# Optimization experiments

Hardware: AMD Instinct MI355X
Metric: run time of the kernel (lower is better)

Reference implementation:

```python
import jax, jax.numpy as jnp
import numpy as np

B, S, D, H = 2, 2048, 1024, 16
DK = D // H
ROPE_BASE = 10000


def _rope_tables(seq_len, dim):
    # RotaryEmbedding.__call__: freqs [S, dim/2], emb = concat([freqs, freqs]) -> [S, dim]
    inv_freq = 1.0 / (ROPE_BASE ** (jnp.arange(0, dim, 2, dtype=jnp.float32) / dim))
    t = jnp.arange(seq_len, dtype=jnp.float32)
    freqs = jnp.outer(t, inv_freq)
    emb = jnp.concatenate([freqs, freqs], axis=-1)
    return jnp.cos(emb), jnp.sin(emb)


def _apply_rope(x, cos, sin):
    # Faithful to apply_rotary_pos_emb: interleaved even/odd channel rotation
    cos = cos[None, None, :, :]  # [1,1,S,DK]
    sin = sin[None, None, :, :]
    x1 = x[..., 0::2]
    x2 = x[..., 1::2]
    r1 = x1 * cos[..., 0::2] - x2 * sin[..., 1::2]
    r2 = x1 * sin[..., 0::2] + x2 * cos[..., 1::2]
    return jnp.stack([r1, r2], axis=-1).reshape(x.shape)


def setup_inputs() -> dict:
    key = jax.random.key(0)
    ks = jax.random.split(key, 11)
    xavier = lambda k: jax.random.uniform(k, (D, D), jnp.float32,
                                          -jnp.sqrt(6.0 / (D + D)), jnp.sqrt(6.0 / (D + D)))
    return {
        "query": jax.random.normal(ks[0], (B, S, D), jnp.float32),
        "key": jax.random.normal(ks[1], (B, S, D), jnp.float32),
        "value": jax.random.normal(ks[2], (B, S, D), jnp.float32),
        "Wq": xavier(ks[3]), "bq": jnp.zeros((D,), jnp.float32),
        "Wk": xavier(ks[4]), "bk": jnp.zeros((D,), jnp.float32),
        "Wv": xavier(ks[5]), "bv": jnp.zeros((D,), jnp.float32),
        "Wo": xavier(ks[6]), "bo": jnp.zeros((D,), jnp.float32),
    }


def reference(query, key, value, Wq, bq, Wk, bk, Wv, bv, Wo, bo):
    def split_heads(x):  # [B,S,D] -> [B,H,S,DK]
        return x.reshape(B, S, H, DK).transpose(0, 2, 1, 3)

    q = split_heads(query @ Wq + bq)
    k = split_heads(key @ Wk + bk)
    v = split_heads(value @ Wv + bv)

    cos, sin = _rope_tables(S, DK)
    q = _apply_rope(q, cos, sin)
    k = _apply_rope(k, cos, sin)

    scores = jnp.einsum("bhqd,bhkd->bhqk", q, k) / jnp.sqrt(jnp.float32(DK))
    causal = jnp.tril(jnp.ones((S, S), dtype=bool))
    scores = jnp.where(causal, scores, jnp.float32(-1e10))
    attn = jax.nn.softmax(scores, axis=-1)
    out = jnp.einsum("bhqk,bhkd->bhqd", attn, v)  # [B,H,S,DK]
    out = out.transpose(0, 2, 1, 3).reshape(B, S, D)
    return out @ Wo + bo
```

## Files before the change

### kernel.cpp

```cpp
#include <hip/hip_runtime.h>
#include <hip/hip_bf16.h>
#include <math.h>

#define B_ 2
#define S_ 2048
#define D_ 1024
#define H_ 16
#define DK_ 64

#define ROPE_C 0.4152410118609203f
#define LOG2E 1.4426950408889634f
#define QSCALE 0.18033688011112042f

typedef float f4 __attribute__((ext_vector_type(4)));
typedef short s8 __attribute__((ext_vector_type(8)));

__device__ __forceinline__ ushort f2b(float f) {
  union { float f; uint u; } v; v.f = f;
  uint u = v.u + 0x7fffu + ((v.u >> 16) & 1u);
  return (ushort)(u >> 16);
}

__device__ __forceinline__ float b2f(ushort u) {
  union { uint u; float f; } v; v.u = ((uint)u) << 16;
  return v.f;
}

__device__ __forceinline__ uint cvtpk(float a, float b) {
  uint r;
  asm("v_cvt_pk_bf16_f32 %0, %1, %2" : "=v"(r) : "v"(a), "v"(b));
  return r;
}

__device__ __forceinline__ void async16(const ushort* g, ushort* l) {
  __builtin_amdgcn_global_load_lds(
      (const __attribute__((address_space(1))) uint*)g,
      (__attribute__((address_space(3))) uint*)l, 16, 0, 0);
}

__global__ __launch_bounds__(256) void prep_all(
    const float* __restrict__ q_in, const float* __restrict__ k_in,
    const float* __restrict__ v_in,
    ushort* __restrict__ Xbq, ushort* __restrict__ Xbk, ushort* __restrict__ Xbv,
    const float* __restrict__ Wq, const float* __restrict__ Wk,
    const float* __restrict__ Wv, const float* __restrict__ Wo,
    ushort* __restrict__ Wtqkv, ushort* __restrict__ Wto) {
  __shared__ ushort T[64][65];
  const int bid = blockIdx.x, t = threadIdx.x;
  if (bid < 6144) {
    const int m = bid >> 11;
    const float* in = (m == 0) ? q_in : (m == 1) ? k_in : v_in;
    ushort* out = (m == 0) ? Xbq : (m == 1) ? Xbk : Xbv;
    int idx = ((bid & 2047) * 256 + t) * 8;
    float4 a = *(const float4*)&in[idx];
    float4 b = *(const float4*)&in[idx + 4];
    ushort tmp[8] = {f2b(a.x), f2b(a.y), f2b(a.z), f2b(a.w),
                     f2b(b.x), f2b(b.y), f2b(b.z), f2b(b.w)};
    *(uint4*)&out[idx] = *(uint4*)tmp;
  } else {
    const int tb = bid - 6144;
    const int m = tb >> 8;
    const float* W = (m == 0) ? Wq : (m == 1) ? Wk : (m == 2) ? Wv : Wo;
    ushort* Wt = (m == 3) ? Wto : Wtqkv + (size_t)m * 1024 * 1024;
    const int k0 = (tb & 15) * 64, n0 = ((tb >> 4) & 15) * 64;
    #pragma unroll
    for (int i = 0; i < 16; ++i) {
      int e = t + i * 256, r = e >> 6, c = e & 63;
      T[c][r] = f2b(W[(size_t)(k0 + r) * D_ + n0 + c]);
    }
    __syncthreads();
    #pragma unroll
    for (int i = 0; i < 16; ++i) {
      int e = t + i * 256, r = e >> 6, c = e & 63;
      Wt[(size_t)(n0 + r) * D_ + k0 + c] = T[r][c];
    }
  }
}

template <int MODE>
__global__ __launch_bounds__(256) void gemm_mfma(
    const ushort* __restrict__ A0, const ushort* __restrict__ A1,
    const ushort* __restrict__ A2, const ushort* __restrict__ Bt,
    const float* __restrict__ bb0, const float* __restrict__ bb1,
    const float* __restrict__ bb2,
    ushort* __restrict__ oq, ushort* __restrict__ ok, ushort* __restrict__ ov,
    float* __restrict__ oo) {
  __shared__ __align__(16) ushort SM[16384];
  ushort* Es = SM;

  const int t = threadIdx.x, w = t >> 6, l = t & 63;
  const int m0 = blockIdx.x * 128, n0 = blockIdx.y * 128;
  const int wm = (w >> 1) * 64, wn = (w & 1) * 64;
  const int lm = l & 15, q4 = (l >> 4) * 4;
  const int hb = l >> 4;

  const ushort* A;
  const float* bias;
  int mat = 0;
  if constexpr (MODE == 0) {
    mat = n0 >> 10;
    A = (mat == 0) ? A0 : (mat == 1) ? A1 : A2;
    bias = (mat == 0) ? bb0 : (mat == 1) ? bb1 : bb2;
  } else {
    A = A0; bias = bb0;
  }

  const int srow = w * 32 + (l >> 2);
  const int pb = l & 3;
  const int lb = pb ^ (srow & 3);
  const ushort* gA = A + (size_t)(m0 + srow) * D_ + lb * 8;
  const ushort* gB = Bt + (size_t)(n0 + srow) * D_ + lb * 8;

#define GSTAGE(bf, kk)                                   \
  {                                                      \
    ushort* lA = SM + (bf) * 4096 + w * 1024;            \
    ushort* lB = SM + 8192 + (bf) * 4096 + w * 1024;     \
    async16(gA + (kk), lA);                              \
    async16(gA + 16 * D_ + (kk), lA + 512);              \
    async16(gB + (kk), lB);                              \
    async16(gB + 16 * D_ + (kk), lB + 512);              \
  }

  f4 acc[4][4];
  #pragma unroll
  for (int i = 0; i < 4; ++i)
    #pragma unroll
    for (int j = 0; j < 4; ++j) acc[i][j] = (f4){0.f, 0.f, 0.f, 0.f};

  GSTAGE(0, 0);
  __syncthreads();

  for (int k0 = 0; k0 < D_; k0 += 32) {
    const int bf = (k0 >> 5) & 1;
    if (k0 + 32 < D_) GSTAGE(bf ^ 1, k0 + 32);
    const ushort* Asb = SM + bf * 4096;
    const ushort* Bsb = SM + 8192 + bf * 4096;
    s8 af[4], bfr[4];
    #pragma unroll
    for (int mt = 0; mt < 4; ++mt) {
      int ra = wm + mt * 16 + lm;
      af[mt] = *(const s8*)&Asb[ra * 32 + ((hb ^ (ra & 3)) << 3)];
    }
    #pragma unroll
    for (int nt = 0; nt < 4; ++nt) {
      int rb = wn + nt * 16 + lm;
      bfr[nt] = *(const s8*)&Bsb[rb * 32 + ((hb ^ (rb & 3)) << 3)];
    }
    __builtin_amdgcn_s_setprio(1);
    #pragma unroll
    for (int mt = 0; mt < 4; ++mt)
      #pragma unroll
      for (int nt = 0; nt < 4; ++nt)
        acc[mt][nt] = __builtin_amdgcn_mfma_f32_16x16x32_bf16(af[mt], bfr[nt], acc[mt][nt], 0, 0, 0);
    __builtin_amdgcn_s_setprio(0);
    __syncthreads();
  }

  if constexpr (MODE == 2) {
    float* Ef = (float*)SM;
    #pragma unroll
    for (int p = 0; p < 2; ++p) {
      if ((w >> 1) == p) {
        #pragma unroll
        for (int nt = 0; nt < 4; ++nt) {
          int col = wn + nt * 16 + lm;
          float bv = bias[n0 + col];
          #pragma unroll
          for (int mt = 0; mt < 4; ++mt)
            #pragma unroll
            for (int r = 0; r < 4; ++r)
              Ef[(mt * 16 + q4 + r) * 128 + col] = acc[mt][nt][r] + bv;
        }
      }
      __syncthreads();
      #pragma unroll
      for (int i = 0; i < 8; ++i) {
        int e = t + i * 256;
        int row = e >> 5, c4 = e & 31;
        *(float4*)&oo[(size_t)(m0 + p * 64 + row) * D_ + n0 + c4 * 4] =
            *(const float4*)&Ef[row * 128 + c4 * 4];
      }
      __syncthreads();
    }
  } else {
    const int nm0 = n0 & 1023;
    const int bI = m0 >> 11;
    if (mat < 2) {
      ushort* dst = (mat == 0) ? oq : ok;
      const float scale = (mat == 0) ? QSCALE : 1.f;
      #pragma unroll
      for (int p = 0; p < 2; ++p) {
        if ((w >> 1) == p) {
          #pragma unroll
          for (int nt = 0; nt < 4; ++nt) {
            int col = wn + nt * 16 + lm;
            float bv = bias[nm0 + col];
            #pragma unroll
            for (int mt = 0; mt < 4; ++mt)
              #pragma unroll
              for (int r = 0; r < 4; ++r)
                Es[(mt * 16 + q4 + r) * 144 + col] = f2b(acc[mt][nt][r] + bv);
          }
        }
        __syncthreads();
        #pragma unroll
        for (int i = 0; i < 4; ++i) {
          int e = t + i * 256, row = e >> 4, ch = e & 15;
          int sg = m0 + p * 64 + row;
          int s = sg & 2047;
          int dcol = nm0 + ch * 8;
          int hh = dcol >> 6, dk0 = dcol & 63;
          ushort xr[8];
          *(uint4*)xr = *(const uint4*)&Es[row * 144 + ch * 8];
          float x[8];
          #pragma unroll
          for (int j = 0; j < 8; ++j) x[j] = b2f(xr[j]);
          const float pos = (float)s;
          ushort o[8];
          #pragma unroll
          for (int j = 0; j < 8; j += 2) {
            int dg = dk0 + j;
            float inve = exp2f(-(float)(dg & 31) * ROPE_C);
            float invo = exp2f(-(float)((dg + 1) & 31) * ROPE_C);
            float se, ce, so, co;
            __sincosf(pos * inve, &se, &ce);
            __sincosf(pos * invo, &so, &co);
            float ev = x[j] * ce - x[j + 1] * so;
            float od = x[j] * se + x[j + 1] * co;
            o[j] = f2b(ev * scale);
            o[j + 1] = f2b(od * scale);
          }
          size_t didx = ((size_t)((bI * 16 + hh) * S_ + s)) * DK_ + dk0;
          *(uint4*)&dst[didx] = *(const uint4*)o;
        }
        __syncthreads();
      }
    } else {
      #pragma unroll
      for (int p = 0; p < 2; ++p) {
        if ((w >> 1) == p) {
          #pragma unroll
          for (int nt = 0; nt < 4; ++nt) {
            int col = wn + nt * 16 + lm;
            float bv = bias[nm0 + col];
            #pragma unroll
            for (int mt = 0; mt < 4; ++mt)
              #pragma unroll
              for (int r = 0; r < 4; ++r)
                Es[col * 72 + (mt * 16 + q4 + r)] = f2b(acc[mt][nt][r] + bv);
          }
        }
        __syncthreads();
        #pragma unroll
        for (int i = 0; i < 4; ++i) {
          int e = t + i * 256, d = e >> 3, sc = e & 7;
          int dcol = nm0 + d;
          int hh = dcol >> 6, dkv = dcol & 63;
          int sg = m0 + p * 64 + sc * 8;
          int s = sg & 2047;
          size_t didx = ((size_t)((bI * 16 + hh) * DK_ + dkv)) * S_ + s;
          *(uint4*)&ov[didx] = *(const uint4*)&Es[d * 72 + sc * 8];
        }
        __syncthreads();
      }
    }
  }
#undef GSTAGE
}

__global__ __launch_bounds__(256, 4) void attn_mfma(const ushort* __restrict__ qf,
                                                    const ushort* __restrict__ kf,
                                                    const ushort* __restrict__ vtf,
                                                    ushort* __restrict__ ctx) {
  __shared__ ushort Ks[2][4096];
  __shared__ ushort Vs[2][4096];
  __shared__ ushort PsS[4096];

  const int t = threadIdx.x, w = t >> 6, l = t & 63;
  const int bid = blockIdx.x;
  const int g = bid >> 8, i = bid & 255, u = i >> 5;
  const int bh = i & 31;
  const int qt = (g == 0) ? (31 - u) : (g == 1) ? u : (g == 2) ? (23 - u) : (8 + u);
  const int i0 = qt * 64;
  const int lm = l & 15, hb = l >> 4, h8 = hb * 8, q4 = hb * 4, w16 = w * 16;
  const size_t base = (size_t)bh * S_ * DK_;
  const int b = bh >> 4, h = bh & 15;

  const int sr = l >> 3, pbk = l & 7;
  const int swS = (pbk ^ sr) << 3;
  const ushort* gkA = kf + base + (size_t)(w * 16 + sr) * DK_ + swS;
  const ushort* gkB = kf + base + (size_t)(w * 16 + sr + 8) * DK_ + swS;
  const ushort* gvA = vtf + base + (size_t)(w * 16 + sr) * S_ + swS;
  const ushort* gvB = vtf + base + (size_t)(w * 16 + sr + 8) * S_ + swS;

#define STAGE(bf, j0)                                       \
  {                                                         \
    ushort* lk = &Ks[bf][w * 1024];                         \
    ushort* lv = &Vs[bf][w * 1024];                         \
    async16(gkA + (size_t)(j0) * DK_, lk);                  \
    async16(gkB + (size_t)(j0) * DK_, lk + 512);            \
    async16(gvA + (j0), lv);                                \
    async16(gvB + (j0), lv + 512);                          \
  }

  const ushort* qp = qf + base + (size_t)(i0 + w16 + lm) * DK_ + h8;
  const s8 bq0 = *(const s8*)qp;
  const s8 bq1 = *(const s8*)(qp + 32);

  const int swr = lm & 7;
  const int cA = (hb ^ swr) << 3;
  const int cB = ((hb + 4) ^ swr) << 3;
  const int prow = (w16 + lm) * 64;

  STAGE(0, 0);

  f4 O[4];
  #pragma unroll
  for (int i2 = 0; i2 < 4; ++i2) O[i2] = (f4){0.f, 0.f, 0.f, 0.f};
  float m_ = -1e30f, l_ = 0.f;

  __syncthreads();

  for (int jt = 0; jt <= qt; ++jt) {
    const int cur = jt & 1;
    if (jt < qt) STAGE(cur ^ 1, (jt + 1) * 64);
    const ushort* Kb = Ks[cur];
    const ushort* Vb = Vs[cur];

    f4 st[4];
    __builtin_amdgcn_s_setprio(1);
    #pragma unroll
    for (int nt = 0; nt < 4; ++nt) {
      const ushort* kRow = Kb + (nt * 16 + lm) * 64;
      s8 a0 = *(const s8*)&kRow[cA];
      s8 a1 = *(const s8*)&kRow[cB];
      f4 a = (f4){0.f, 0.f, 0.f, 0.f};
      a = __builtin_amdgcn_mfma_f32_16x16x32_bf16(a0, bq0, a, 0, 0, 0);
      a = __builtin_amdgcn_mfma_f32_16x16x32_bf16(a1, bq1, a, 0, 0, 0);
      st[nt] = a;
    }
    __builtin_amdgcn_s_setprio(0);

    if (jt == qt) {
      #pragma unroll
      for (int nt = 0; nt < 4; ++nt)
        #pragma unroll
        for (int r = 0; r < 4; ++r)
          if (nt * 16 + q4 + r > w16 + lm) st[nt][r] = -1e30f;
    }

    float x0 = fmaxf(fmaxf(st[0][0], st[0][1]), fmaxf(st[0][2], st[0][3]));
    float x1 = fmaxf(fmaxf(st[1][0], st[1][1]), fmaxf(st[1][2], st[1][3]));
    float x2 = fmaxf(fmaxf(st[2][0], st[2][1]), fmaxf(st[2][2], st[2][3]));
    float x3 = fmaxf(fmaxf(st[3][0], st[3][1]), fmaxf(st[3][2], st[3][3]));
    float pm = fmaxf(fmaxf(x0, x1), fmaxf(x2, x3));
    pm = fmaxf(pm, __shfl_xor(pm, 16));
    pm = fmaxf(pm, __shfl_xor(pm, 32));

    const bool stable = __all(pm <= m_ + 4.0f);
    float mn = m_, alpha = 1.f;
    if (!stable) {
      mn = fmaxf(m_, pm);
      alpha = exp2f(m_ - mn);
      m_ = mn;
    }

    #pragma unroll
    for (int nt = 0; nt < 4; ++nt)
      #pragma unroll
      for (int r = 0; r < 4; ++r)
        st[nt][r] = exp2f(st[nt][r] - mn);
    float s0 = (st[0][0] + st[0][1]) + (st[0][2] + st[0][3]);
    float s1 = (st[1][0] + st[1][1]) + (st[1][2] + st[1][3]);
    float s2 = (st[2][0] + st[2][1]) + (st[2][2] + st[2][3]);
    float s3 = (st[3][0] + st[3][1]) + (st[3][2] + st[3][3]);
    float ps = (s0 + s1) + (s2 + s3);
    ps += __shfl_xor(ps, 16);
    ps += __shfl_xor(ps, 32);

    if (stable) {
      l_ += ps;
    } else {
      l_ = l_ * alpha + ps;
      float ar[4];
      #pragma unroll
      for (int r = 0; r < 4; ++r) ar[r] = __shfl(alpha, q4 + r);
      #pragma unroll
      for (int nt = 0; nt < 4; ++nt)
        #pragma unroll
        for (int r = 0; r < 4; ++r) O[nt][r] *= ar[r];
    }

    #pragma unroll
    for (int nt = 0; nt < 4; ++nt) {
      uint2 pp;
      pp.x = cvtpk(st[nt][0], st[nt][1]);
      pp.y = cvtpk(st[nt][2], st[nt][3]);
      const int pidx = prow + ((((nt << 1) + (hb >> 1)) ^ swr) << 3) + ((hb & 1) << 2);
      *(uint2*)&PsS[pidx] = pp;
    }
    s8 ap0 = *(const s8*)&PsS[prow + cA];
    s8 ap1 = *(const s8*)&PsS[prow + cB];

    __builtin_amdgcn_s_setprio(1);
    #pragma unroll
    for (int nt = 0; nt < 4; ++nt) {
      const ushort* vRow = Vb + (nt * 16 + lm) * 64;
      s8 v0 = *(const s8*)&vRow[cA];
      s8 v1 = *(const s8*)&vRow[cB];
      O[nt] = __builtin_amdgcn_mfma_f32_16x16x32_bf16(ap0, v0, O[nt], 0, 0, 0);
      O[nt] = __builtin_amdgcn_mfma_f32_16x16x32_bf16(ap1, v1, O[nt], 0, 0, 0);
    }
    __builtin_amdgcn_s_setprio(0);

    __syncthreads();
  }

  float il[4];
  #pragma unroll
  for (int r = 0; r < 4; ++r) il[r] = 1.f / __shfl(l_, q4 + r);
  #pragma unroll
  for (int nt = 0; nt < 4; ++nt)
    #pragma unroll
    for (int r = 0; r < 4; ++r) {
      int row = w16 + q4 + r, col = nt * 16 + lm;
      PsS[row * 64 + ((((col >> 3) ^ (row & 7)) << 3)) + (col & 7)] =
          f2b(O[nt][r] * il[r]);
    }
  __syncthreads();
  #pragma unroll
  for (int i2 = 0; i2 < 2; ++i2) {
    int e = t + i2 * 256, row = e >> 3, ch = e & 7;
    int s = i0 + row;
    *(uint4*)&ctx[((size_t)(b * S_ + s)) * D_ + h * 64 + ch * 8] =
        *(const uint4*)&PsS[row * 64 + ((ch ^ (row & 7)) << 3)];
  }
#undef STAGE
}

extern "C" void kernel_launch(void* const* d_in, const int* in_sizes, int n_in,
                              void* d_out, int out_size, void* d_ws, size_t ws_size,
                              hipStream_t stream) {
  const float* q_in = (const float*)d_in[0];
  const float* k_in = (const float*)d_in[1];
  const float* v_in = (const float*)d_in[2];
  const float* Wq = (const float*)d_in[3];
  const float* bq = (const float*)d_in[4];
  const float* Wk = (const float*)d_in[5];
  const float* bk = (const float*)d_in[6];
  const float* Wv = (const float*)d_in[7];
  const float* bv = (const float*)d_in[8];
  const float* Wo = (const float*)d_in[9];
  const float* bo = (const float*)d_in[10];

  const size_t NE = (size_t)B_ * S_ * D_;
  ushort* Xbq = (ushort*)d_ws;
  ushort* Xbk = Xbq + NE;
  ushort* Xbv = Xbk + NE;
  ushort* Wtqkv = Xbv + NE;
  ushort* Wto = Wtqkv + 3 * 1024 * 1024;
  ushort* qfb = Wto + 1024 * 1024;
  ushort* kfb = qfb + NE;
  ushort* vtb = kfb + NE;
  ushort* ctxb = vtb + NE;

  prep_all<<<7168, 256, 0, stream>>>(q_in, k_in, v_in, Xbq, Xbk, Xbv,
                                     Wq, Wk, Wv, Wo, Wtqkv, Wto);

  gemm_mfma<0><<<dim3(32, 24), 256, 0, stream>>>(
      Xbq, Xbk, Xbv, Wtqkv, bq, bk, bv, qfb, kfb, vtb, nullptr);

  attn_mfma<<<1024, 256, 0, stream>>>(qfb, kfb, vtb, ctxb);

  gemm_mfma<2><<<dim3(32, 8), 256, 0, stream>>>(
      ctxb, ctxb, ctxb, Wto, bo, bo, bo, nullptr, nullptr, nullptr,
      (float*)d_out);
}
```

Measured before the change: 220.4 us.

## Process two 64-row query tiles per attention block to reuse K/V loads

Each attention block now handles 128 query rows (two 64-row sub-tiles A and B) of one head, sharing each staged K/V tile across both sub-tiles' MFMAs. The grid shrinks from 1024 to 512 blocks, launch bounds drop to 2 blocks per SM, and the old balanced qt permutation is replaced by a simple reversed 2D grid. This halves K/V global and LDS staging traffic per query row but doubles register use and removes the load-balanced tile ordering, which may cost occupancy and tail balance.

Measured after the change: 247.4 us. +12.3%, slower.

```diff
diff --git a/kernel.cpp b/kernel.cpp
--- a/kernel.cpp
+++ b/kernel.cpp
@@ -268,20 +268,18 @@
 #undef GSTAGE
 }
 
-__global__ __launch_bounds__(256, 4) void attn_mfma(const ushort* __restrict__ qf,
+__global__ __launch_bounds__(256, 2) void attn_mfma(const ushort* __restrict__ qf,
                                                     const ushort* __restrict__ kf,
                                                     const ushort* __restrict__ vtf,
                                                     ushort* __restrict__ ctx) {
   __shared__ ushort Ks[2][4096];
   __shared__ ushort Vs[2][4096];
-  __shared__ ushort PsS[4096];
+  __shared__ ushort PsS[8192];
 
   const int t = threadIdx.x, w = t >> 6, l = t & 63;
-  const int bid = blockIdx.x;
-  const int g = bid >> 8, i = bid & 255, u = i >> 5;
-  const int bh = i & 31;
-  const int qt = (g == 0) ? (31 - u) : (g == 1) ? u : (g == 2) ? (23 - u) : (8 + u);
-  const int i0 = qt * 64;
+  const int bh = blockIdx.x;
+  const int p = 15 - (int)blockIdx.y;
+  const int i0 = p * 128;
   const int lm = l & 15, hb = l >> 4, h8 = hb * 8, q4 = hb * 4, w16 = w * 16;
   const size_t base = (size_t)bh * S_ * DK_;
   const int b = bh >> 4, h = bh & 15;
@@ -303,104 +301,180 @@
     async16(gvB + (j0), lv + 512);                          \
   }
 
-  const ushort* qp = qf + base + (size_t)(i0 + w16 + lm) * DK_ + h8;
-  const s8 bq0 = *(const s8*)qp;
-  const s8 bq1 = *(const s8*)(qp + 32);
+  const ushort* qpA = qf + base + (size_t)(i0 + w16 + lm) * DK_ + h8;
+  const ushort* qpB = qpA + (size_t)64 * DK_;
+  const s8 bqA0 = *(const s8*)qpA;
+  const s8 bqA1 = *(const s8*)(qpA + 32);
+  const s8 bqB0 = *(const s8*)qpB;
+  const s8 bqB1 = *(const s8*)(qpB + 32);
 
   const int swr = lm & 7;
   const int cA = (hb ^ swr) << 3;
   const int cB = ((hb + 4) ^ swr) << 3;
-  const int prow = (w16 + lm) * 64;
+  const int prowA = (w16 + lm) * 64;
+  const int prowB = (64 + w16 + lm) * 64;
 
   STAGE(0, 0);
 
-  f4 O[4];
+  f4 OA[4], OB[4];
   #pragma unroll
-  for (int i2 = 0; i2 < 4; ++i2) O[i2] = (f4){0.f, 0.f, 0.f, 0.f};
-  float m_ = -1e30f, l_ = 0.f;
+  for (int i = 0; i < 4; ++i) {
+    OA[i] = (f4){0.f, 0.f, 0.f, 0.f};
+    OB[i] = (f4){0.f, 0.f, 0.f, 0.f};
+  }
+  float mA_ = -1e30f, lA_ = 0.f;
+  float mB_ = -1e30f, lB_ = 0.f;
 
   __syncthreads();
 
-  for (int jt = 0; jt <= qt; ++jt) {
+  const int jlast = 2 * p + 1;
+  for (int jt = 0; jt <= jlast; ++jt) {
     const int cur = jt & 1;
-    if (jt < qt) STAGE(cur ^ 1, (jt + 1) * 64);
+    if (jt < jlast) STAGE(cur ^ 1, (jt + 1) * 64);
     const ushort* Kb = Ks[cur];
     const ushort* Vb = Vs[cur];
-
-    f4 st[4];
+    const bool doA = (jt < jlast);
+
+    f4 stA[4], stB[4];
     __builtin_amdgcn_s_setprio(1);
     #pragma unroll
     for (int nt = 0; nt < 4; ++nt) {
       const ushort* kRow = Kb + (nt * 16 + lm) * 64;
       s8 a0 = *(const s8*)&kRow[cA];
       s8 a1 = *(const s8*)&kRow[cB];
-      f4 a = (f4){0.f, 0.f, 0.f, 0.f};
-      a = __builtin_amdgcn_mfma_f32_16x16x32_bf16(a0, bq0, a, 0, 0, 0);
-      a = __builtin_amdgcn_mfma_f32_16x16x32_bf16(a1, bq1, a, 0, 0, 0);
-      st[nt] = a;
+      f4 sb = (f4){0.f, 0.f, 0.f, 0.f};
+      sb = __builtin_amdgcn_mfma_f32_16x16x32_bf16(a0, bqB0, sb, 0, 0, 0);
+      sb = __builtin_amdgcn_mfma_f32_16x16x32_bf16(a1, bqB1, sb, 0, 0, 0);
+      stB[nt] = sb;
+      if (doA) {
+        f4 sa = (f4){0.f, 0.f, 0.f, 0.f};
+        sa = __builtin_amdgcn_mfma_f32_16x16x32_bf16(a0, bqA0, sa, 0, 0, 0);
+        sa = __builtin_amdgcn_mfma_f32_16x16x32_bf16(a1, bqA1, sa, 0, 0, 0);
+        stA[nt] = sa;
+      }
     }
     __builtin_amdgcn_s_setprio(0);
 
-    if (jt == qt) {
+    if (jt == 2 * p) {
       #pragma unroll
       for (int nt = 0; nt < 4; ++nt)
         #pragma unroll
         for (int r = 0; r < 4; ++r)
-          if (nt * 16 + q4 + r > w16 + lm) st[nt][r] = -1e30f;
-    }
-
-    float x0 = fmaxf(fmaxf(st[0][0], st[0][1]), fmaxf(st[0][2], st[0][3]));
-    float x1 = fmaxf(fmaxf(st[1][0], st[1][1]), fmaxf(st[1][2], st[1][3]));
-    float x2 = fmaxf(fmaxf(st[2][0], st[2][1]), fmaxf(st[2][2], st[2][3]));
-    float x3 = fmaxf(fmaxf(st[3][0], st[3][1]), fmaxf(st[3][2], st[3][3]));
-    float pm = fmaxf(fmaxf(x0, x1), fmaxf(x2, x3));
-    pm = fmaxf(pm, __shfl_xor(pm, 16));
-    pm = fmaxf(pm, __shfl_xor(pm, 32));
-
-    const bool stable = __all(pm <= m_ + 4.0f);
-    float mn = m_, alpha = 1.f;
-    if (!stable) {
-      mn = fmaxf(m_, pm);
-      alpha = exp2f(m_ - mn);
-      m_ = mn;
-    }
-
-    #pragma unroll
-    for (int nt = 0; nt < 4; ++nt)
-      #pragma unroll
-      for (int r = 0; r < 4; ++r)
-        st[nt][r] = exp2f(st[nt][r] - mn);
-    float s0 = (st[0][0] + st[0][1]) + (st[0][2] + st[0][3]);
-    float s1 = (st[1][0] + st[1][1]) + (st[1][2] + st[1][3]);
-    float s2 = (st[2][0] + st[2][1]) + (st[2][2] + st[2][3]);
-    float s3 = (st[3][0] + st[3][1]) + (st[3][2] + st[3][3]);
-    float ps = (s0 + s1) + (s2 + s3);
-    ps += __shfl_xor(ps, 16);
-    ps += __shfl_xor(ps, 32);
-
-    if (stable) {
-      l_ += ps;
-    } else {
-      l_ = l_ * alpha + ps;
-      float ar[4];
-      #pragma unroll
-      for (int r = 0; r < 4; ++r) ar[r] = __shfl(alpha, q4 + r);
+          if (nt * 16 + q4 + r > w16 + lm) stA[nt][r] = -1e30f;
+    }
+    if (jt == jlast) {
       #pragma unroll
       for (int nt = 0; nt < 4; ++nt)
         #pragma unroll
-        for (int r = 0; r < 4; ++r) O[nt][r] *= ar[r];
-    }
-
-    #pragma unroll
-    for (int nt = 0; nt < 4; ++nt) {
-      uint2 pp;
-      pp.x = cvtpk(st[nt][0], st[nt][1]);
-      pp.y = cvtpk(st[nt][2], st[nt][3]);
-      const int pidx = prow + ((((nt << 1) + (hb >> 1)) ^ swr) << 3) + ((hb & 1) << 2);
-      *(uint2*)&PsS[pidx] = pp;
-    }
-    s8 ap0 = *(const s8*)&PsS[prow + cA];
-    s8 ap1 = *(const s8*)&PsS[prow + cB];
+        for (int r = 0; r < 4; ++r)
+          if (nt * 16 + q4 + r > w16 + lm) stB[nt][r] = -1e30f;
+    }
+
+    if (doA) {
+      float x0 = fmaxf(fmaxf(stA[0][0], stA[0][1]), fmaxf(stA[0][2], stA[0][3]));
+      float x1 = fmaxf(fmaxf(stA[1][0], stA[1][1]), fmaxf(stA[1][2], stA[1][3]));
+      float x2 = fmaxf(fmaxf(stA[2][0], stA[2][1]), fmaxf(stA[2][2], stA[2][3]));
+      float x3 = fmaxf(fmaxf(stA[3][0], stA[3][1]), fmaxf(stA[3][2], stA[3][3]));
+      float pm = fmaxf(fmaxf(x0, x1), fmaxf(x2, x3));
+      pm = fmaxf(pm, __shfl_xor(pm, 16));
+      pm = fmaxf(pm, __shfl_xor(pm, 32));
+      const bool stable = __all(pm <= mA_ + 4.0f);
+      float mn = mA_, alpha = 1.f;
+      if (!stable) {
+        mn = fmaxf(mA_, pm);
+        alpha = exp2f(mA_ - mn);
+        mA_ = mn;
+      }
+      #pragma unroll
+      for (int nt = 0; nt < 4; ++nt)
+        #pragma unroll
+        for (int r = 0; r < 4; ++r)
+          stA[nt][r] = exp2f(stA[nt][r] - mn);
+      float s0 = (stA[0][0] + stA[0][1]) + (stA[0][2] + stA[0][3]);
+      float s1 = (stA[1][0] + stA[1][1]) + (stA[1][2] + stA[1][3]);
+      float s2 = (stA[2][0] + stA[2][1]) + (stA[2][2] + stA[2][3]);
+      float s3 = (stA[3][0] + stA[3][1]) + (stA[3][2] + stA[3][3]);
+      float ps = (s0 + s1) + (s2 + s3);
+      ps += __shfl_xor(ps, 16);
+      ps += __shfl_xor(ps, 32);
+      if (stable) {
+        lA_ += ps;
+      } else {
+        lA_ = lA_ * alpha + ps;
+        float ar[4];
+        #pragma unroll
+        for (int r = 0; r < 4; ++r) ar[r] = __shfl(alpha, q4 + r);
+        #pragma unroll
+        for (int nt = 0; nt < 4; ++nt)
+          #pragma unroll
+          for (int r = 0; r < 4; ++r) OA[nt][r] *= ar[r];
+      }
+      #pragma unroll
+      for (int nt = 0; nt < 4; ++nt) {
+        uint2 pp;
+        pp.x = cvtpk(stA[nt][0], stA[nt][1]);
+        pp.y = cvtpk(stA[nt][2], stA[nt][3]);
+        const int pidx = prowA + ((((nt << 1) + (hb >> 1)) ^ swr) << 3) + ((hb & 1) << 2);
+        *(uint2*)&PsS[pidx] = pp;
+      }
+    }
+
+    {
+      float x0 = fmaxf(fmaxf(stB[0][0], stB[0][1]), fmaxf(stB[0][2], stB[0][3]));
+      float x1 = fmaxf(fmaxf(stB[1][0], stB[1][1]), fmaxf(stB[1][2], stB[1][3]));
+      float x2 = fmaxf(fmaxf(stB[2][0], stB[2][1]), fmaxf(stB[2][2], stB[2][3]));
+      float x3 = fmaxf(fmaxf(stB[3][0], stB[3][1]), fmaxf(stB[3][2], stB[3][3]));
+      float pm = fmaxf(fmaxf(x0, x1), fmaxf(x2, x3));
+      pm = fmaxf(pm, __shfl_xor(pm, 16));
+      pm = fmaxf(pm, __shfl_xor(pm, 32));
+      const bool stable = __all(pm <= mB_ + 4.0f);
+      float mn = mB_, alpha = 1.f;
+      if (!stable) {
+        mn = fmaxf(mB_, pm);
+        alpha = exp2f(mB_ - mn);
+        mB_ = mn;
+      }
+      #pragma unroll
+      for (int nt = 0; nt < 4; ++nt)
+        #pragma unroll
+        for (int r = 0; r < 4; ++r)
+          stB[nt][r] = exp2f(stB[nt][r] - mn);
+      float s0 = (stB[0][0] + stB[0][1]) + (stB[0][2] + stB[0][3]);
+      float s1 = (stB[1][0] + stB[1][1]) + (stB[1][2] + stB[1][3]);
+      float s2 = (stB[2][0] + stB[2][1]) + (stB[2][2] + stB[2][3]);
+      float s3 = (stB[3][0] + stB[3][1]) + (stB[3][2] + stB[3][3]);
+      float ps = (s0 + s1) + (s2 + s3);
+      ps += __shfl_xor(ps, 16);
+      ps += __shfl_xor(ps, 32);
+      if (stable) {
+        lB_ += ps;
+      } else {
+        lB_ = lB_ * alpha + ps;
+        float ar[4];
+        #pragma unroll
+        for (int r = 0; r < 4; ++r) ar[r] = __shfl(alpha, q4 + r);
+        #pragma unroll
+        for (int nt = 0; nt < 4; ++nt)
+          #pragma unroll
+          for (int r = 0; r < 4; ++r) OB[nt][r] *= ar[r];
+      }
+      #pragma unroll
+      for (int nt = 0; nt < 4; ++nt) {
+        uint2 pp;
+        pp.x = cvtpk(stB[nt][0], stB[nt][1]);
+        pp.y = cvtpk(stB[nt][2], stB[nt][3]);
+        const int pidx = prowB + ((((nt << 1) + (hb >> 1)) ^ swr) << 3) + ((hb & 1) << 2);
+        *(uint2*)&PsS[pidx] = pp;
+      }
+    }
+
+    s8 apA0, apA1;
+    if (doA) {
+      apA0 = *(const s8*)&PsS[prowA + cA];
+      apA1 = *(const s8*)&PsS[prowA + cB];
+    }
+    s8 apB0 = *(const s8*)&PsS[prowB + cA];
+    s8 apB1 = *(const s8*)&PsS[prowB + cB];
 
     __builtin_amdgcn_s_setprio(1);
     #pragma unroll
@@ -408,29 +482,39 @@
       const ushort* vRow = Vb + (nt * 16 + lm) * 64;
       s8 v0 = *(const s8*)&vRow[cA];
       s8 v1 = *(const s8*)&vRow[cB];
-      O[nt] = __builtin_amdgcn_mfma_f32_16x16x32_bf16(ap0, v0, O[nt], 0, 0, 0);
-      O[nt] = __builtin_amdgcn_mfma_f32_16x16x32_bf16(ap1, v1, O[nt], 0, 0, 0);
+      if (doA) {
+        OA[nt] = __builtin_amdgcn_mfma_f32_16x16x32_bf16(apA0, v0, OA[nt], 0, 0, 0);
+        OA[nt] = __builtin_amdgcn_mfma_f32_16x16x32_bf16(apA1, v1, OA[nt], 0, 0, 0);
+      }
+      OB[nt] = __builtin_amdgcn_mfma_f32_16x16x32_bf16(apB0, v0, OB[nt], 0, 0, 0);
+      OB[nt] = __builtin_amdgcn_mfma_f32_16x16x32_bf16(apB1, v1, OB[nt], 0, 0, 0);
     }
     __builtin_amdgcn_s_setprio(0);
 
     __syncthreads();
   }
 
-  float il[4];
+  float ilA[4], ilB[4];
   #pragma unroll
-  for (int r = 0; r < 4; ++r) il[r] = 1.f / __shfl(l_, q4 + r);
+  for (int r = 0; r < 4; ++r) {
+    ilA[r] = 1.f / __shfl(lA_, q4 + r);
+    ilB[r] = 1.f / __shfl(lB_, q4 + r);
+  }
   #pragma unroll
   for (int nt = 0; nt < 4; ++nt)
     #pragma unroll
     for (int r = 0; r < 4; ++r) {
-      int row = w16 + q4 + r, col = nt * 16 + lm;
-      PsS[row * 64 + ((((col >> 3) ^ (row & 7)) << 3)) + (col & 7)] =
-          f2b(O[nt][r] * il[r]);
+      int rowA = w16 + q4 + r, col = nt * 16 + lm;
+      PsS[rowA * 64 + (((col >> 3) ^ (rowA & 7)) << 3) + (col & 7)] =
+          f2b(OA[nt][r] * ilA[r]);
+      int rowB = rowA + 64;
+      PsS[rowB * 64 + (((col >> 3) ^ (rowB & 7)) << 3) + (col & 7)] =
+          f2b(OB[nt][r] * ilB[r]);
     }
   __syncthreads();
   #pragma unroll
-  for (int i2 = 0; i2 < 2; ++i2) {
-    int e = t + i2 * 256, row = e >> 3, ch = e & 7;
+  for (int i = 0; i < 4; ++i) {
+    int e = t + i * 256, row = e >> 3, ch = e & 7;
     int s = i0 + row;
     *(uint4*)&ctx[((size_t)(b * S_ + s)) * D_ + h * 64 + ch * 8] =
         *(const uint4*)&PsS[row * 64 + ((ch ^ (row & 7)) << 3)];
@@ -470,7 +554,7 @@
   gemm_mfma<0><<<dim3(32, 24), 256, 0, stream>>>(
       Xbq, Xbk, Xbv, Wtqkv, bq, bk, bv, qfb, kfb, vtb, nullptr);
 
-  attn_mfma<<<1024, 256, 0, stream>>>(qfb, kfb, vtb, ctxb);
+  attn_mfma<<<dim3(32, 16), 256, 0, stream>>>(qfb, kfb, vtb, ctxb);
 
   gemm_mfma<2><<<dim3(32, 8), 256, 0, stream>>>(
       ctxb, ctxb, ctxb, Wto, bo, bo, bo, nullptr, nullptr, nullptr,
```

## Precompute RoPE cos/sin table and simplify attention block scheduling

Applied to the files above, without the earlier changes.

Adds extra blocks to the prep kernel that fill a per-position cos/sin table in workspace. The QKV GEMM epilogue then reads this table instead of computing exp2 and sincos per element. Separately, the attention kernel drops its interleaved grid mapping that balanced causal work across groups and uses a plain 2D grid ordered by descending query tile. The table adds global memory traffic, and the simpler ordering may change how load is balanced across CUs.

After: 223.4 us. Within noise of the previous version (+1.3%).

```diff
diff --git a/kernel.cpp b/kernel.cpp
--- a/kernel.cpp
+++ b/kernel.cpp
@@ -44,7 +44,8 @@
     ushort* __restrict__ Xbq, ushort* __restrict__ Xbk, ushort* __restrict__ Xbv,
     const float* __restrict__ Wq, const float* __restrict__ Wk,
     const float* __restrict__ Wv, const float* __restrict__ Wo,
-    ushort* __restrict__ Wtqkv, ushort* __restrict__ Wto) {
+    ushort* __restrict__ Wtqkv, ushort* __restrict__ Wto,
+    float* __restrict__ rtab) {
   __shared__ ushort T[64][65];
   const int bid = blockIdx.x, t = threadIdx.x;
   if (bid < 6144) {
@@ -57,7 +58,7 @@
     ushort tmp[8] = {f2b(a.x), f2b(a.y), f2b(a.z), f2b(a.w),
                      f2b(b.x), f2b(b.y), f2b(b.z), f2b(b.w)};
     *(uint4*)&out[idx] = *(uint4*)tmp;
-  } else {
+  } else if (bid < 7168) {
     const int tb = bid - 6144;
     const int m = tb >> 8;
     const float* W = (m == 0) ? Wq : (m == 1) ? Wk : (m == 2) ? Wv : Wo;
@@ -74,6 +75,15 @@
       int e = t + i * 256, r = e >> 6, c = e & 63;
       Wt[(size_t)(n0 + r) * D_ + k0 + c] = T[r][c];
     }
+  } else {
+    const int tb2 = bid - 7168;
+    const int s = tb2 * 8 + (t >> 5), f = t & 31;
+    float invf = exp2f(-(float)f * ROPE_C);
+    float ang = (float)s * invf;
+    float2 cs2;
+    cs2.x = cosf(ang);
+    cs2.y = sinf(ang);
+    *(float2*)&rtab[(size_t)s * 64 + f * 2] = cs2;
   }
 }
 
@@ -84,7 +94,7 @@
     const float* __restrict__ bb0, const float* __restrict__ bb1,
     const float* __restrict__ bb2,
     ushort* __restrict__ oq, ushort* __restrict__ ok, ushort* __restrict__ ov,
-    float* __restrict__ oo) {
+    float* __restrict__ oo, const float* __restrict__ rtab) {
   __shared__ __align__(16) ushort SM[16384];
   ushort* Es = SM;
 
@@ -212,21 +222,16 @@
           int hh = dcol >> 6, dk0 = dcol & 63;
           ushort xr[8];
           *(uint4*)xr = *(const uint4*)&Es[row * 144 + ch * 8];
-          float x[8];
+          const float2* tr = (const float2*)&rtab[(size_t)s * 64 + (dk0 & 31) * 2];
+          float2 tv[8];
           #pragma unroll
-          for (int j = 0; j < 8; ++j) x[j] = b2f(xr[j]);
-          const float pos = (float)s;
+          for (int j = 0; j < 8; ++j) tv[j] = tr[j];
           ushort o[8];
           #pragma unroll
           for (int j = 0; j < 8; j += 2) {
-            int dg = dk0 + j;
-            float inve = exp2f(-(float)(dg & 31) * ROPE_C);
-            float invo = exp2f(-(float)((dg + 1) & 31) * ROPE_C);
-            float se, ce, so, co;
-            __sincosf(pos * inve, &se, &ce);
-            __sincosf(pos * invo, &so, &co);
-            float ev = x[j] * ce - x[j + 1] * so;
-            float od = x[j] * se + x[j + 1] * co;
+            float xe = b2f(xr[j]), xo = b2f(xr[j + 1]);
+            float ev = xe * tv[j].x - xo * tv[j + 1].y;
+            float od = xe * tv[j].y + xo * tv[j + 1].x;
             o[j] = f2b(ev * scale);
             o[j + 1] = f2b(od * scale);
           }
@@ -277,10 +282,7 @@
   __shared__ ushort PsS[4096];
 
   const int t = threadIdx.x, w = t >> 6, l = t & 63;
-  const int bid = blockIdx.x;
-  const int g = bid >> 8, i = bid & 255, u = i >> 5;
-  const int bh = i & 31;
-  const int qt = (g == 0) ? (31 - u) : (g == 1) ? u : (g == 2) ? (23 - u) : (8 + u);
+  const int bh = blockIdx.x, qt = 31 - (int)blockIdx.y;
   const int i0 = qt * 64;
   const int lm = l & 15, hb = l >> 4, h8 = hb * 8, q4 = hb * 4, w16 = w * 16;
   const size_t base = (size_t)bh * S_ * DK_;
@@ -316,7 +318,7 @@
 
   f4 O[4];
   #pragma unroll
-  for (int i2 = 0; i2 < 4; ++i2) O[i2] = (f4){0.f, 0.f, 0.f, 0.f};
+  for (int i = 0; i < 4; ++i) O[i] = (f4){0.f, 0.f, 0.f, 0.f};
   float m_ = -1e30f, l_ = 0.f;
 
   __syncthreads();
@@ -429,8 +431,8 @@
     }
   __syncthreads();
   #pragma unroll
-  for (int i2 = 0; i2 < 2; ++i2) {
-    int e = t + i2 * 256, row = e >> 3, ch = e & 7;
+  for (int i = 0; i < 2; ++i) {
+    int e = t + i * 256, row = e >> 3, ch = e & 7;
     int s = i0 + row;
     *(uint4*)&ctx[((size_t)(b * S_ + s)) * D_ + h * 64 + ch * 8] =
         *(const uint4*)&PsS[row * 64 + ((ch ^ (row & 7)) << 3)];
@@ -463,16 +465,17 @@
   ushort* kfb = qfb + NE;
   ushort* vtb = kfb + NE;
   ushort* ctxb = vtb + NE;
-
-  prep_all<<<7168, 256, 0, stream>>>(q_in, k_in, v_in, Xbq, Xbk, Xbv,
-                                     Wq, Wk, Wv, Wo, Wtqkv, Wto);
+  float* rtab = (float*)(ctxb + NE);
+
+  prep_all<<<7424, 256, 0, stream>>>(q_in, k_in, v_in, Xbq, Xbk, Xbv,
+                                     Wq, Wk, Wv, Wo, Wtqkv, Wto, rtab);
 
   gemm_mfma<0><<<dim3(32, 24), 256, 0, stream>>>(
-      Xbq, Xbk, Xbv, Wtqkv, bq, bk, bv, qfb, kfb, vtb, nullptr);
-
-  attn_mfma<<<1024, 256, 0, stream>>>(qfb, kfb, vtb, ctxb);
+      Xbq, Xbk, Xbv, Wtqkv, bq, bk, bv, qfb, kfb, vtb, nullptr, rtab);
+
+  attn_mfma<<<dim3(32, 32), 256, 0, stream>>>(qfb, kfb, vtb, ctxb);
 
   gemm_mfma<2><<<dim3(32, 8), 256, 0, stream>>>(
       ctxb, ctxb, ctxb, Wto, bo, bo, bo, nullptr, nullptr, nullptr,
-      (float*)d_out);
-}
+      (float*)d_out, nullptr);
+}
```

## Fuse fp32-to-bf16 activation conversion into QKV GEMM A-tile loads

Applied to the files above, without the earlier changes.

The QKV projection GEMM now reads fp32 activations directly from global memory into registers, converts them to bf16 with packed cvt instructions, and writes them to LDS after the MFMA loop. This removes the separate conversion pass and its bf16 workspace round trip. The catch is that A loads become synchronous register loads instead of async LDS DMA, which costs registers and latency hiding. Separately, the attention grid is simplified from an interleaved balanced mapping to a 2D grid ordered by descending query tile.

Measured after the change: 241.6 us. +9.6%, slower.

```diff
diff --git a/kernel.cpp b/kernel.cpp
--- a/kernel.cpp
+++ b/kernel.cpp
@@ -39,48 +39,33 @@
 }
 
 __global__ __launch_bounds__(256) void prep_all(
-    const float* __restrict__ q_in, const float* __restrict__ k_in,
-    const float* __restrict__ v_in,
-    ushort* __restrict__ Xbq, ushort* __restrict__ Xbk, ushort* __restrict__ Xbv,
     const float* __restrict__ Wq, const float* __restrict__ Wk,
     const float* __restrict__ Wv, const float* __restrict__ Wo,
     ushort* __restrict__ Wtqkv, ushort* __restrict__ Wto) {
   __shared__ ushort T[64][65];
   const int bid = blockIdx.x, t = threadIdx.x;
-  if (bid < 6144) {
-    const int m = bid >> 11;
-    const float* in = (m == 0) ? q_in : (m == 1) ? k_in : v_in;
-    ushort* out = (m == 0) ? Xbq : (m == 1) ? Xbk : Xbv;
-    int idx = ((bid & 2047) * 256 + t) * 8;
-    float4 a = *(const float4*)&in[idx];
-    float4 b = *(const float4*)&in[idx + 4];
-    ushort tmp[8] = {f2b(a.x), f2b(a.y), f2b(a.z), f2b(a.w),
-                     f2b(b.x), f2b(b.y), f2b(b.z), f2b(b.w)};
-    *(uint4*)&out[idx] = *(uint4*)tmp;
-  } else {
-    const int tb = bid - 6144;
-    const int m = tb >> 8;
-    const float* W = (m == 0) ? Wq : (m == 1) ? Wk : (m == 2) ? Wv : Wo;
-    ushort* Wt = (m == 3) ? Wto : Wtqkv + (size_t)m * 1024 * 1024;
-    const int k0 = (tb & 15) * 64, n0 = ((tb >> 4) & 15) * 64;
-    #pragma unroll
-    for (int i = 0; i < 16; ++i) {
-      int e = t + i * 256, r = e >> 6, c = e & 63;
-      T[c][r] = f2b(W[(size_t)(k0 + r) * D_ + n0 + c]);
-    }
-    __syncthreads();
-    #pragma unroll
-    for (int i = 0; i < 16; ++i) {
-      int e = t + i * 256, r = e >> 6, c = e & 63;
-      Wt[(size_t)(n0 + r) * D_ + k0 + c] = T[r][c];
-    }
+  const int m = bid >> 8;
+  const float* W = (m == 0) ? Wq : (m == 1) ? Wk : (m == 2) ? Wv : Wo;
+  ushort* Wt = (m == 3) ? Wto : Wtqkv + (size_t)m * 1024 * 1024;
+  const int k0 = (bid & 15) * 64, n0 = ((bid >> 4) & 15) * 64;
+  #pragma unroll
+  for (int i = 0; i < 16; ++i) {
+    int e = t + i * 256, r = e >> 6, c = e & 63;
+    T[c][r] = f2b(W[(size_t)(k0 + r) * D_ + n0 + c]);
+  }
+  __syncthreads();
+  #pragma unroll
+  for (int i = 0; i < 16; ++i) {
+    int e = t + i * 256, r = e >> 6, c = e & 63;
+    Wt[(size_t)(n0 + r) * D_ + k0 + c] = T[r][c];
   }
 }
 
 template <int MODE>
 __global__ __launch_bounds__(256) void gemm_mfma(
-    const ushort* __restrict__ A0, const ushort* __restrict__ A1,
-    const ushort* __restrict__ A2, const ushort* __restrict__ Bt,
+    const float* __restrict__ Af0, const float* __restrict__ Af1,
+    const float* __restrict__ Af2, const ushort* __restrict__ Ab,
+    const ushort* __restrict__ Bt,
     const float* __restrict__ bb0, const float* __restrict__ bb1,
     const float* __restrict__ bb2,
     ushort* __restrict__ oq, ushort* __restrict__ ok, ushort* __restrict__ ov,
@@ -94,31 +79,59 @@
   const int lm = l & 15, q4 = (l >> 4) * 4;
   const int hb = l >> 4;
 
-  const ushort* A;
   const float* bias;
   int mat = 0;
+  const float* A32 = nullptr;
   if constexpr (MODE == 0) {
     mat = n0 >> 10;
-    A = (mat == 0) ? A0 : (mat == 1) ? A1 : A2;
+    A32 = (mat == 0) ? Af0 : (mat == 1) ? Af1 : Af2;
     bias = (mat == 0) ? bb0 : (mat == 1) ? bb1 : bb2;
   } else {
-    A = A0; bias = bb0;
+    bias = bb0;
   }
 
   const int srow = w * 32 + (l >> 2);
   const int pb = l & 3;
   const int lb = pb ^ (srow & 3);
-  const ushort* gA = A + (size_t)(m0 + srow) * D_ + lb * 8;
   const ushort* gB = Bt + (size_t)(n0 + srow) * D_ + lb * 8;
-
-#define GSTAGE(bf, kk)                                   \
+  const float* gAf = nullptr;
+  const ushort* gA = nullptr;
+  if constexpr (MODE == 0) {
+    gAf = A32 + (size_t)(m0 + srow) * D_ + pb * 8;
+  } else {
+    gA = Ab + (size_t)(m0 + srow) * D_ + lb * 8;
+  }
+
+#define BSTAGE(bf, kk)                                   \
+  {                                                      \
+    ushort* lB = SM + 8192 + (bf) * 4096 + w * 1024;     \
+    async16(gB + (kk), lB);                              \
+    async16(gB + 16 * D_ + (kk), lB + 512);              \
+  }
+#define ASTAGE_DMA(bf, kk)                               \
   {                                                      \
     ushort* lA = SM + (bf) * 4096 + w * 1024;            \
-    ushort* lB = SM + 8192 + (bf) * 4096 + w * 1024;     \
     async16(gA + (kk), lA);                              \
     async16(gA + 16 * D_ + (kk), lA + 512);              \
-    async16(gB + (kk), lB);                              \
-    async16(gB + 16 * D_ + (kk), lB + 512);              \
+  }
+  float4 pa0, pa1, pa2, pa3;
+#define ALOAD(kk)                                        \
+  {                                                      \
+    pa0 = *(const float4*)&gAf[(kk)];                    \
+    pa1 = *(const float4*)&gAf[(kk) + 4];                \
+    pa2 = *(const float4*)&gAf[16 * D_ + (kk)];          \
+    pa3 = *(const float4*)&gAf[16 * D_ + (kk) + 4];      \
+  }
+#define AWRITE(bf)                                       \
+  {                                                      \
+    ushort* lA = SM + (bf) * 4096;                       \
+    uint4 w0, w1;                                        \
+    w0.x = cvtpk(pa0.x, pa0.y); w0.y = cvtpk(pa0.z, pa0.w); \
+    w0.z = cvtpk(pa1.x, pa1.y); w0.w = cvtpk(pa1.z, pa1.w); \
+    w1.x = cvtpk(pa2.x, pa2.y); w1.y = cvtpk(pa2.z, pa2.w); \
+    w1.z = cvtpk(pa3.x, pa3.y); w1.w = cvtpk(pa3.z, pa3.w); \
+    *(uint4*)&lA[srow * 32 + (lb << 3)] = w0;            \
+    *(uint4*)&lA[(srow + 16) * 32 + (lb << 3)] = w1;     \
   }
 
   f4 acc[4][4];
@@ -127,12 +140,24 @@
     #pragma unroll
     for (int j = 0; j < 4; ++j) acc[i][j] = (f4){0.f, 0.f, 0.f, 0.f};
 
-  GSTAGE(0, 0);
+  if constexpr (MODE == 0) {
+    ALOAD(0);
+    AWRITE(0);
+    BSTAGE(0, 0);
+  } else {
+    ASTAGE_DMA(0, 0);
+    BSTAGE(0, 0);
+  }
   __syncthreads();
 
   for (int k0 = 0; k0 < D_; k0 += 32) {
     const int bf = (k0 >> 5) & 1;
-    if (k0 + 32 < D_) GSTAGE(bf ^ 1, k0 + 32);
+    const bool more = (k0 + 32 < D_);
+    if constexpr (MODE == 0) {
+      if (more) { ALOAD(k0 + 32); BSTAGE(bf ^ 1, k0 + 32); }
+    } else {
+      if (more) { ASTAGE_DMA(bf ^ 1, k0 + 32); BSTAGE(bf ^ 1, k0 + 32); }
+    }
     const ushort* Asb = SM + bf * 4096;
     const ushort* Bsb = SM + 8192 + bf * 4096;
     s8 af[4], bfr[4];
@@ -153,6 +178,9 @@
       for (int nt = 0; nt < 4; ++nt)
         acc[mt][nt] = __builtin_amdgcn_mfma_f32_16x16x32_bf16(af[mt], bfr[nt], acc[mt][nt], 0, 0, 0);
     __builtin_amdgcn_s_setprio(0);
+    if constexpr (MODE == 0) {
+      if (more) AWRITE(bf ^ 1);
+    }
     __syncthreads();
   }
 
@@ -265,7 +293,10 @@
       }
     }
   }
-#undef GSTAGE
+#undef BSTAGE
+#undef ASTAGE_DMA
+#undef ALOAD
+#undef AWRITE
 }
 
 __global__ __launch_bounds__(256, 4) void attn_mfma(const ushort* __restrict__ qf,
@@ -277,10 +308,7 @@
   __shared__ ushort PsS[4096];
 
   const int t = threadIdx.x, w = t >> 6, l = t & 63;
-  const int bid = blockIdx.x;
-  const int g = bid >> 8, i = bid & 255, u = i >> 5;
-  const int bh = i & 31;
-  const int qt = (g == 0) ? (31 - u) : (g == 1) ? u : (g == 2) ? (23 - u) : (8 + u);
+  const int bh = blockIdx.x, qt = 31 - (int)blockIdx.y;
   const int i0 = qt * 64;
   const int lm = l & 15, hb = l >> 4, h8 = hb * 8, q4 = hb * 4, w16 = w * 16;
   const size_t base = (size_t)bh * S_ * DK_;
@@ -316,7 +344,7 @@
 
   f4 O[4];
   #pragma unroll
-  for (int i2 = 0; i2 < 4; ++i2) O[i2] = (f4){0.f, 0.f, 0.f, 0.f};
+  for (int i = 0; i < 4; ++i) O[i] = (f4){0.f, 0.f, 0.f, 0.f};
   float m_ = -1e30f, l_ = 0.f;
 
   __syncthreads();
@@ -429,8 +457,8 @@
     }
   __syncthreads();
   #pragma unroll
-  for (int i2 = 0; i2 < 2; ++i2) {
-    int e = t + i2 * 256, row = e >> 3, ch = e & 7;
+  for (int i = 0; i < 2; ++i) {
+    int e = t + i * 256, row = e >> 3, ch = e & 7;
     int s = i0 + row;
     *(uint4*)&ctx[((size_t)(b * S_ + s)) * D_ + h * 64 + ch * 8] =
         *(const uint4*)&PsS[row * 64 + ((ch ^ (row & 7)) << 3)];
@@ -454,25 +482,21 @@
   const float* bo = (const float*)d_in[10];
 
   const size_t NE = (size_t)B_ * S_ * D_;
-  ushort* Xbq = (ushort*)d_ws;
-  ushort* Xbk = Xbq + NE;
-  ushort* Xbv = Xbk + NE;
-  ushort* Wtqkv = Xbv + NE;
+  ushort* Wtqkv = (ushort*)d_ws;
   ushort* Wto = Wtqkv + 3 * 1024 * 1024;
   ushort* qfb = Wto + 1024 * 1024;
   ushort* kfb = qfb + NE;
   ushort* vtb = kfb + NE;
   ushort* ctxb = vtb + NE;
 
-  prep_all<<<7168, 256, 0, stream>>>(q_in, k_in, v_in, Xbq, Xbk, Xbv,
-                                     Wq, Wk, Wv, Wo, Wtqkv, Wto);
+  prep_all<<<1024, 256, 0, stream>>>(Wq, Wk, Wv, Wo, Wtqkv, Wto);
 
   gemm_mfma<0><<<dim3(32, 24), 256, 0, stream>>>(
-      Xbq, Xbk, Xbv, Wtqkv, bq, bk, bv, qfb, kfb, vtb, nullptr);
-
-  attn_mfma<<<1024, 256, 0, stream>>>(qfb, kfb, vtb, ctxb);
+      q_in, k_in, v_in, nullptr, Wtqkv, bq, bk, bv, qfb, kfb, vtb, nullptr);
+
+  attn_mfma<<<dim3(32, 32), 256, 0, stream>>>(qfb, kfb, vtb, ctxb);
 
   gemm_mfma<2><<<dim3(32, 8), 256, 0, stream>>>(
-      ctxb, ctxb, ctxb, Wto, bo, bo, bo, nullptr, nullptr, nullptr,
-      (float*)d_out);
-}
+      nullptr, nullptr, nullptr, ctxb, Wto, bo, bo, bo, nullptr, nullptr,
+      nullptr, (float*)d_out);
+}
```
